# Kernel tuning notes

Measured on AMD Instinct MI355X. Metric: run time of the kernel, lower is better.

The kernel has to match this reference:

```python
import jax, jax.numpy as jnp
import numpy as np

IN_DIM, HID_DIM, OUT_DIM = 1024, 2048, 1024
DEG1, DEG2 = 8, 8
BATCH = 16384


def cheby_kan_layer(x, coeffs):
    """x: [b, i]; coeffs: [i, o, d+1] -> [b, o].
    Per-feature min-max normalize over batch to [-1,1], Chebyshev recurrence, contract."""
    degree = coeffs.shape[-1] - 1
    mn = jnp.min(x, axis=0, keepdims=True)
    mx = jnp.max(x, axis=0, keepdims=True)
    x = 2.0 * (x - mn) / (mx - mn) - 1.0
    Ts = [jnp.ones_like(x)]
    if degree > 0:
        Ts.append(x)
    for _ in range(2, degree + 1):
        Ts.append(2.0 * x * Ts[-1] - Ts[-2])
    cheby = jnp.stack(Ts, axis=-1)  # [b, i, d+1]
    return jnp.einsum('bid,iod->bo', cheby, coeffs)


def setup_inputs() -> dict:
    key = jax.random.key(0)
    k1, k2, k3 = jax.random.split(key, 3)
    x = jax.random.normal(k1, (BATCH, IN_DIM), dtype=jnp.float32)
    # kaiming-uniform-ish init for coeffs
    b1 = float(np.sqrt(6.0 / IN_DIM))
    b2 = float(np.sqrt(6.0 / HID_DIM))
    coeffs1 = jax.random.uniform(k2, (IN_DIM, HID_DIM, DEG1 + 1), dtype=jnp.float32, minval=-b1, maxval=b1)
    coeffs2 = jax.random.uniform(k3, (HID_DIM, OUT_DIM, DEG2 + 1), dtype=jnp.float32, minval=-b2, maxval=b2)
    return {"x": x, "coeffs1": coeffs1, "coeffs2": coeffs2}


def reference(x, coeffs1, coeffs2):
    h = cheby_kan_layer(x, coeffs1)
    y = cheby_kan_layer(h, coeffs2)
    return y
```

## Files before the change

### kernel.cpp

```cpp
#include <hip/hip_runtime.h>
#include <hip/hip_bf16.h>
#include <stdint.h>


constexpr int BATCH   = 16384;
constexpr int IN_DIM  = 1024;
constexpr int HID_DIM = 2048;
constexpr int OUT_DIM = 1024;
#define DP1 9

using bf16_t = __hip_bfloat16;

typedef __attribute__((ext_vector_type(4))) float f32x4;
typedef __attribute__((ext_vector_type(8))) short s16x8;
typedef __attribute__((ext_vector_type(16))) float f32x16;
typedef __attribute__((ext_vector_type(16))) __bf16 bf16x16;

static __device__ __forceinline__ unsigned int f2bf_u(float f) {
  union { __hip_bfloat16 h; unsigned short u; } cv;
  cv.h = __float2bfloat16(f);
  return (unsigned int)cv.u;
}

template <typename T>
__global__ void kan_minmax_partial(const T* __restrict__ x, int rows, int cols,
                                   float* __restrict__ mnp, float* __restrict__ mxp) {
  const int c  = blockIdx.x * 64 + (threadIdx.x & 63);
  const int rg = threadIdx.x >> 6;
  const int P  = gridDim.y;
  const int chunk = rows / P;
  const int r0 = blockIdx.y * chunk;
  float mn = 1e30f, mx = -1e30f;
  for (int r = r0 + rg; r < r0 + chunk; r += 4) {
    float v = (float)x[(size_t)r * cols + c];
    mn = fminf(mn, v); mx = fmaxf(mx, v);
  }
  __shared__ float smn[256], smx[256];
  smn[threadIdx.x] = mn; smx[threadIdx.x] = mx;
  __syncthreads();
  if (rg == 0) {
    int t = threadIdx.x;
    mn = fminf(fminf(smn[t], smn[t + 64]), fminf(smn[t + 128], smn[t + 192]));
    mx = fmaxf(fmaxf(smx[t], smx[t + 64]), fmaxf(smx[t + 128], smx[t + 192]));
    mnp[(size_t)blockIdx.y * cols + c] = mn;
    mxp[(size_t)blockIdx.y * cols + c] = mx;
  }
}

__global__ void kan_minmax_finalize(const float* __restrict__ mnp, const float* __restrict__ mxp,
                                    int cols, int P, float* __restrict__ s, float* __restrict__ t) {
  int c = blockIdx.x * blockDim.x + threadIdx.x;
  if (c >= cols) return;
  float mn = 1e30f, mx = -1e30f;
  for (int p = 0; p < P; ++p) {
    mn = fminf(mn, mnp[(size_t)p * cols + c]);
    mx = fmaxf(mx, mxp[(size_t)p * cols + c]);
  }
  float inv = 2.0f / (mx - mn);
  s[c] = inv;
  t[c] = -mn * inv - 1.0f;
}

__global__ void kan_repack(const float* __restrict__ coeffs, int I, int O,
                           bf16_t* __restrict__ Bp) {
  const int NIB = I / 32;
  const int ib = blockIdx.x % NIB;
  const int ntile = blockIdx.x / NIB;
  const size_t slab0 = (size_t)(ntile * NIB + ib) * 9 * 8192;
  for (int c = threadIdx.x; c < 1024; c += 256) {
    const int l16  = c & 15;
    const int quad = (c >> 4) & 3;
    const int ng   = c >> 6;
    const int o = ntile * 256 + ng * 16 + l16;
    const int ibase = ib * 32 + quad * 8;
    float v[8][9];
#pragma unroll
    for (int q = 0; q < 8; ++q) {
      const float* rp = coeffs + ((size_t)(ibase + q) * O + o) * DP1;
#pragma unroll
      for (int d = 0; d < 9; ++d) v[q][d] = rp[d];
    }
#pragma unroll
    for (int d = 0; d < 9; ++d) {
      unsigned int pk[4];
#pragma unroll
      for (int q = 0; q < 4; ++q)
        pk[q] = f2bf_u(v[2 * q][d]) | (f2bf_u(v[2 * q + 1][d]) << 16);
      *reinterpret_cast<uint4*>(reinterpret_cast<char*>(Bp) +
          (slab0 + (size_t)d * 8192 + (size_t)c * 8) * 2) =
          make_uint4(pk[0], pk[1], pk[2], pk[3]);
    }
  }
}

template <typename AT, typename OT>
__launch_bounds__(256, 2)
__global__ void kan_cheby_gemm(const AT* __restrict__ X, const bf16_t* __restrict__ Bp,
                               const float* __restrict__ sc, const float* __restrict__ tc,
                               OT* __restrict__ out, int I, int N) {
  __shared__ __align__(16) short Als[2][4096];
  __shared__ __align__(16) short Bls[2][8192];

  const int m0   = blockIdx.x * 128;
  const int tid  = threadIdx.x;
  const int lane = tid & 63;
  const int wave = tid >> 6;
  const int wr   = wave >> 1;
  const int wc   = wave & 1;
  const int wm4  = wr * 4;
  const int wn16 = wc * 8;
  const int quad = lane >> 4;
  const int l16  = lane & 15;

  const int ma = tid & 127;
  const int hf = tid >> 7;

  const int NIB = I / 32;
  const int nstage = NIB * 9;
  const size_t slab_base = (size_t)blockIdx.y * NIB * 9 * 8192;

  auto dma_b = [&](int ss) {
    const char* g = reinterpret_cast<const char*>(Bp + slab_base + (size_t)ss * 8192) +
                    wave * 4096 + lane * 16;
    char* l = reinterpret_cast<char*>(&Bls[ss & 1][0]) + wave * 4096;
#pragma unroll
    for (int t = 0; t < 4; ++t)
      __builtin_amdgcn_global_load_lds(
          (const __attribute__((address_space(1))) void*)(g + t * 1024),
          (__attribute__((address_space(3))) void*)(l + t * 1024), 16, 0, 0);
  };

  uint4 rq[4];
  auto load_raw = [&](int ibx) {
    const char* xp = reinterpret_cast<const char*>(
        X + (size_t)(m0 + ma) * I + ibx * 32 + hf * 16);
    if constexpr (sizeof(AT) == 4) {
      rq[0] = *reinterpret_cast<const uint4*>(xp +  0);
      rq[1] = *reinterpret_cast<const uint4*>(xp + 16);
      rq[2] = *reinterpret_cast<const uint4*>(xp + 32);
      rq[3] = *reinterpret_cast<const uint4*>(xp + 48);
    } else {
      rq[0] = *reinterpret_cast<const uint4*>(xp +  0);
      rq[1] = *reinterpret_cast<const uint4*>(xp + 16);
    }
  };

  f32x16 xv, Tm1, Tm2;
#pragma unroll
  for (int j = 0; j < 16; ++j) { xv[j] = 0.f; Tm1[j] = 0.f; Tm2[j] = 0.f; }

  auto unpack_norm = [&](int ibx) {
    const int fbase = ibx * 32 + hf * 16;
    float rv[16];
    const unsigned int* w = reinterpret_cast<const unsigned int*>(rq);
    if constexpr (sizeof(AT) == 4) {
#pragma unroll
      for (int j = 0; j < 16; ++j) rv[j] = __uint_as_float(w[j]);
    } else {
#pragma unroll
      for (int q = 0; q < 8; ++q) {
        rv[2 * q + 0] = __uint_as_float(w[q] << 16);
        rv[2 * q + 1] = __uint_as_float(w[q] & 0xffff0000u);
      }
    }
    const float4* sp = reinterpret_cast<const float4*>(sc + fbase);
    const float4* tp = reinterpret_cast<const float4*>(tc + fbase);
#pragma unroll
    for (int v = 0; v < 4; ++v) {
      float4 s4 = sp[v], t4 = tp[v];
      xv[4 * v + 0] = fmaf(rv[4 * v + 0], s4.x, t4.x);
      xv[4 * v + 1] = fmaf(rv[4 * v + 1], s4.y, t4.y);
      xv[4 * v + 2] = fmaf(rv[4 * v + 2], s4.z, t4.z);
      xv[4 * v + 3] = fmaf(rv[4 * v + 3], s4.w, t4.w);
    }
  };

  auto write_a = [&](int buf, const f32x16& tv) {
    union { bf16x16 v; uint4 q[2]; } u;
    u.v = __builtin_convertvector(tv, bf16x16);
    char* b = reinterpret_cast<char*>(&Als[buf][0]) +
              (ma >> 4) * 1024 + hf * 512 + (ma & 15) * 16;
    *reinterpret_cast<uint4*>(b)       = u.q[0];
    *reinterpret_cast<uint4*>(b + 256) = u.q[1];
  };

  f32x4 acc[4][8] = {};

  load_raw(0);
  dma_b(0);
  {
    f32x16 ones;
#pragma unroll
    for (int j = 0; j < 16; ++j) ones[j] = 1.0f;
    write_a(0, ones);
    Tm1 = ones;
  }
  __syncthreads();

  int dn = 1, ibn = 0;
  for (int s = 0; s < nstage; ++s) {
    if (s + 1 < nstage) {
      dma_b(s + 1);
      f32x16 tv;
      if (dn == 0) {
#pragma unroll
        for (int j = 0; j < 16; ++j) tv[j] = 1.0f;
      } else if (dn == 1) {
        unpack_norm(ibn);
        if (ibn + 1 < NIB) load_raw(ibn + 1);
        tv = xv;
      } else {
        tv = 2.0f * xv * Tm1 - Tm2;
      }
      Tm2 = Tm1; Tm1 = tv;
      write_a((s + 1) & 1, tv);
      if (++dn == DP1) { dn = 0; ++ibn; }
    }

    {
      const char* Ab = reinterpret_cast<const char*>(&Als[s & 1][0]) + lane * 16;
      const char* Bb = reinterpret_cast<const char*>(&Bls[s & 1][0]) + lane * 16;
      s16x8 fa[4], fb[8];
#pragma unroll
      for (int mt = 0; mt < 4; ++mt)
        fa[mt] = *reinterpret_cast<const s16x8*>(Ab + (wm4 + mt) * 1024);
#pragma unroll
      for (int nt = 0; nt < 8; ++nt)
        fb[nt] = *reinterpret_cast<const s16x8*>(Bb + (wn16 + nt) * 1024);
#pragma unroll
      for (int mt = 0; mt < 4; ++mt)
#pragma unroll
        for (int nt = 0; nt < 8; ++nt)
          acc[mt][nt] = __builtin_amdgcn_mfma_f32_16x16x32_bf16(
              fa[mt], fb[nt], acc[mt][nt], 0, 0, 0);
    }

    __syncthreads();
  }

  const int n0 = blockIdx.y * 256;
#pragma unroll
  for (int mt = 0; mt < 4; ++mt) {
#pragma unroll
    for (int nt = 0; nt < 8; ++nt) {
      const int n = n0 + wc * 128 + nt * 16 + l16;
#pragma unroll
      for (int r = 0; r < 4; ++r) {
        const int m = m0 + wr * 64 + mt * 16 + quad * 4 + r;
        float v = acc[mt][nt][r];
        if constexpr (sizeof(OT) == 4)
          out[(size_t)m * N + n] = v;
        else
          out[(size_t)m * N + n] = __float2bfloat16(v);
      }
    }
  }
}

extern "C" void kernel_launch(void* const* d_in, const int* in_sizes, int n_in,
                              void* d_out, int out_size, void* d_ws, size_t ws_size,
                              hipStream_t stream) {
  const float* x  = (const float*)d_in[0];
  const float* c1 = (const float*)d_in[1];
  const float* c2 = (const float*)d_in[2];
  float* out = (float*)d_out;

  char* ws = (char*)d_ws;
  size_t off = 0;
  auto take = [&](size_t n) -> char* {
    char* p = ws + off;
    off += (n + 255) & ~(size_t)255;
    return p;
  };
  bf16_t* Bp1 = (bf16_t*)take((size_t)HID_DIM * IN_DIM  * DP1 * 2);
  bf16_t* Bp2 = (bf16_t*)take((size_t)OUT_DIM * HID_DIM * DP1 * 2);
  bf16_t* h   = (bf16_t*)take((size_t)BATCH * HID_DIM * 2);
  float* s1  = (float*)take(IN_DIM  * 4);
  float* t1  = (float*)take(IN_DIM  * 4);
  float* s2  = (float*)take(HID_DIM * 4);
  float* t2  = (float*)take(HID_DIM * 4);
  float* mnp = (float*)take((size_t)16 * HID_DIM * 4);
  float* mxp = (float*)take((size_t)16 * HID_DIM * 4);

  kan_minmax_partial<float><<<dim3(IN_DIM / 64, 16), 256, 0, stream>>>(x, BATCH, IN_DIM, mnp, mxp);
  kan_minmax_finalize<<<dim3(IN_DIM / 256), 256, 0, stream>>>(mnp, mxp, IN_DIM, 16, s1, t1);
  kan_repack<<<dim3((HID_DIM / 256) * (IN_DIM / 32)), 256, 0, stream>>>(c1, IN_DIM, HID_DIM, Bp1);
  kan_repack<<<dim3((OUT_DIM / 256) * (HID_DIM / 32)), 256, 0, stream>>>(c2, HID_DIM, OUT_DIM, Bp2);
  kan_cheby_gemm<float, bf16_t><<<dim3(BATCH / 128, HID_DIM / 256), 256, 0, stream>>>(
      x, Bp1, s1, t1, h, IN_DIM, HID_DIM);

  kan_minmax_partial<bf16_t><<<dim3(HID_DIM / 64, 16), 256, 0, stream>>>(h, BATCH, HID_DIM, mnp, mxp);
  kan_minmax_finalize<<<dim3(HID_DIM / 256), 256, 0, stream>>>(mnp, mxp, HID_DIM, 16, s2, t2);
  kan_cheby_gemm<bf16_t, float><<<dim3(BATCH / 128, OUT_DIM / 256), 256, 0, stream>>>(
      h, Bp2, s2, t2, out, HID_DIM, OUT_DIM);
}
```

Measured before the change: 1.881 ms.

## Triple-buffer B tiles with deeper prefetch and precise vmcnt waits

Moves the B-tile LDS staging from double to triple buffering, so the async global-to-LDS load is issued two stages ahead. The full __syncthreads is replaced by explicit s_waitcnt vmcnt/lgkmcnt counts plus a raw barrier, so the in-flight prefetch no longer has to drain every stage. MFMA issue priority is also raised around the compute block. This costs extra LDS, which may limit occupancy, and the hand-counted vmcnt values are fragile if the compiler reorders or changes the load counts.

Measured after the change: 2.007 ms. +6.7%, slower.

```diff
diff --git a/kernel.cpp b/kernel.cpp
--- a/kernel.cpp
+++ b/kernel.cpp
@@ -15,6 +15,9 @@
 typedef __attribute__((ext_vector_type(8))) short s16x8;
 typedef __attribute__((ext_vector_type(16))) float f32x16;
 typedef __attribute__((ext_vector_type(16))) __bf16 bf16x16;
+
+#define WAITV(N) asm volatile("s_waitcnt vmcnt(" #N ")" ::: "memory")
+#define WAITL()  asm volatile("s_waitcnt lgkmcnt(0)" ::: "memory")
 
 static __device__ __forceinline__ unsigned int f2bf_u(float f) {
   union { __hip_bfloat16 h; unsigned short u; } cv;
@@ -99,7 +102,7 @@
                                const float* __restrict__ sc, const float* __restrict__ tc,
                                OT* __restrict__ out, int I, int N) {
   __shared__ __align__(16) short Als[2][4096];
-  __shared__ __align__(16) short Bls[2][8192];
+  __shared__ __align__(16) short Bls[3][8192];
 
   const int m0   = blockIdx.x * 128;
   const int tid  = threadIdx.x;
@@ -119,10 +122,10 @@
   const int nstage = NIB * 9;
   const size_t slab_base = (size_t)blockIdx.y * NIB * 9 * 8192;
 
-  auto dma_b = [&](int ss) {
+  auto dma_b = [&](int ss, int buf) {
     const char* g = reinterpret_cast<const char*>(Bp + slab_base + (size_t)ss * 8192) +
                     wave * 4096 + lane * 16;
-    char* l = reinterpret_cast<char*>(&Bls[ss & 1][0]) + wave * 4096;
+    char* l = reinterpret_cast<char*>(&Bls[buf][0]) + wave * 4096;
 #pragma unroll
     for (int t = 0; t < 4; ++t)
       __builtin_amdgcn_global_load_lds(
@@ -187,7 +190,8 @@
   f32x4 acc[4][8] = {};
 
   load_raw(0);
-  dma_b(0);
+  dma_b(0, 0);
+  dma_b(1, 1);
   {
     f32x16 ones;
 #pragma unroll
@@ -195,19 +199,27 @@
     write_a(0, ones);
     Tm1 = ones;
   }
-  __syncthreads();
+  WAITV(4);
+  WAITL();
+  __builtin_amdgcn_s_barrier();
 
   int dn = 1, ibn = 0;
+  int cb = 0, nb = 2;
   for (int s = 0; s < nstage; ++s) {
-    if (s + 1 < nstage) {
-      dma_b(s + 1);
+    const bool have1 = (s + 1 < nstage);
+    const bool have2 = (s + 2 < nstage);
+
+    if (have2) dma_b(s + 2, nb);
+
+    bool did_raw = false;
+    if (have1) {
       f32x16 tv;
       if (dn == 0) {
 #pragma unroll
         for (int j = 0; j < 16; ++j) tv[j] = 1.0f;
       } else if (dn == 1) {
         unpack_norm(ibn);
-        if (ibn + 1 < NIB) load_raw(ibn + 1);
+        if (ibn + 1 < NIB) { load_raw(ibn + 1); did_raw = true; }
         tv = xv;
       } else {
         tv = 2.0f * xv * Tm1 - Tm2;
@@ -219,7 +231,7 @@
 
     {
       const char* Ab = reinterpret_cast<const char*>(&Als[s & 1][0]) + lane * 16;
-      const char* Bb = reinterpret_cast<const char*>(&Bls[s & 1][0]) + lane * 16;
+      const char* Bb = reinterpret_cast<const char*>(&Bls[cb][0]) + lane * 16;
       s16x8 fa[4], fb[8];
 #pragma unroll
       for (int mt = 0; mt < 4; ++mt)
@@ -227,15 +239,31 @@
 #pragma unroll
       for (int nt = 0; nt < 8; ++nt)
         fb[nt] = *reinterpret_cast<const s16x8*>(Bb + (wn16 + nt) * 1024);
+      __builtin_amdgcn_s_setprio(1);
 #pragma unroll
       for (int mt = 0; mt < 4; ++mt)
 #pragma unroll
         for (int nt = 0; nt < 8; ++nt)
           acc[mt][nt] = __builtin_amdgcn_mfma_f32_16x16x32_bf16(
               fa[mt], fb[nt], acc[mt][nt], 0, 0, 0);
-    }
-
-    __syncthreads();
+      __builtin_amdgcn_s_setprio(0);
+    }
+
+    if (have1) {
+      if (have2) {
+        if (did_raw) {
+          if constexpr (sizeof(AT) == 4) WAITV(8); else WAITV(6);
+        } else {
+          WAITV(4);
+        }
+      } else {
+        WAITV(0);
+      }
+      WAITL();
+      __builtin_amdgcn_s_barrier();
+    }
+    cb = (cb == 2) ? 0 : cb + 1;
+    nb = (nb == 2) ? 0 : nb + 1;
   }
 
   const int n0 = blockIdx.y * 256;
```

## Fold degree-0 Chebyshev term into per-output bias to shrink GEMM K

Applied to the files above, without the earlier changes.

The T0=1 term contributes sum_i coeffs[i,o,0] to every output, so the repack kernel now sums those coefficients into a per-output bias and drops degree 0 from the packed B matrix. This cuts the GEMM K dimension from 9 to 8 stages per input block. The bias is added in the epilogue, and the scale/shift vectors are staged in LDS. LDS fragment loads are also hoisted ahead of the A-tile computation. The change adds an extra small reduction kernel, and the bias sum is now in fp32 where it was previously rounded to bf16 per term.

Measured after the change: 1.913 ms. Within noise of the previous version (+1.7%).

```diff
diff --git a/kernel.cpp b/kernel.cpp
--- a/kernel.cpp
+++ b/kernel.cpp
@@ -62,11 +62,12 @@
 }
 
 __global__ void kan_repack(const float* __restrict__ coeffs, int I, int O,
-                           bf16_t* __restrict__ Bp) {
+                           bf16_t* __restrict__ Bp, float* __restrict__ biasp) {
   const int NIB = I / 32;
   const int ib = blockIdx.x % NIB;
   const int ntile = blockIdx.x / NIB;
-  const size_t slab0 = (size_t)(ntile * NIB + ib) * 9 * 8192;
+  const size_t slab0 = (size_t)(ntile * NIB + ib) * 8 * 8192;
+  __shared__ float sb[1024];
   for (int c = threadIdx.x; c < 1024; c += 256) {
     const int l16  = c & 15;
     const int quad = (c >> 4) & 3;
@@ -80,26 +81,50 @@
 #pragma unroll
       for (int d = 0; d < 9; ++d) v[q][d] = rp[d];
     }
-#pragma unroll
-    for (int d = 0; d < 9; ++d) {
+    float bsum = 0.f;
+#pragma unroll
+    for (int q = 0; q < 8; ++q) bsum += v[q][0];
+    sb[c] = bsum;
+#pragma unroll
+    for (int d = 1; d < 9; ++d) {
       unsigned int pk[4];
 #pragma unroll
       for (int q = 0; q < 4; ++q)
         pk[q] = f2bf_u(v[2 * q][d]) | (f2bf_u(v[2 * q + 1][d]) << 16);
       *reinterpret_cast<uint4*>(reinterpret_cast<char*>(Bp) +
-          (slab0 + (size_t)d * 8192 + (size_t)c * 8) * 2) =
+          (slab0 + (size_t)(d - 1) * 8192 + (size_t)c * 8) * 2) =
           make_uint4(pk[0], pk[1], pk[2], pk[3]);
     }
   }
+  __syncthreads();
+  {
+    const int t = threadIdx.x;
+    const int ng = t >> 4, l16 = t & 15;
+    const float s = sb[ng * 64 + l16] + sb[ng * 64 + 16 + l16] +
+                    sb[ng * 64 + 32 + l16] + sb[ng * 64 + 48 + l16];
+    biasp[(size_t)ib * O + ntile * 256 + t] = s;
+  }
+}
+
+__global__ void kan_bias_finalize(const float* __restrict__ biasp, int NIB, int O,
+                                  float* __restrict__ bias) {
+  const int o = blockIdx.x * blockDim.x + threadIdx.x;
+  if (o >= O) return;
+  float s = 0.f;
+  for (int p = 0; p < NIB; ++p) s += biasp[(size_t)p * O + o];
+  bias[o] = s;
 }
 
 template <typename AT, typename OT>
 __launch_bounds__(256, 2)
 __global__ void kan_cheby_gemm(const AT* __restrict__ X, const bf16_t* __restrict__ Bp,
                                const float* __restrict__ sc, const float* __restrict__ tc,
+                               const float* __restrict__ bias,
                                OT* __restrict__ out, int I, int N) {
   __shared__ __align__(16) short Als[2][4096];
   __shared__ __align__(16) short Bls[2][8192];
+  __shared__ __align__(16) float scl[2048];
+  __shared__ __align__(16) float tcl[2048];
 
   const int m0   = blockIdx.x * 128;
   const int tid  = threadIdx.x;
@@ -116,8 +141,8 @@
   const int hf = tid >> 7;
 
   const int NIB = I / 32;
-  const int nstage = NIB * 9;
-  const size_t slab_base = (size_t)blockIdx.y * NIB * 9 * 8192;
+  const int nstage = NIB * 8;
+  const size_t slab_base = (size_t)blockIdx.y * NIB * 8 * 8192;
 
   auto dma_b = [&](int ss) {
     const char* g = reinterpret_cast<const char*>(Bp + slab_base + (size_t)ss * 8192) +
@@ -163,8 +188,8 @@
         rv[2 * q + 1] = __uint_as_float(w[q] & 0xffff0000u);
       }
     }
-    const float4* sp = reinterpret_cast<const float4*>(sc + fbase);
-    const float4* tp = reinterpret_cast<const float4*>(tc + fbase);
+    const float4* sp = reinterpret_cast<const float4*>(&scl[fbase]);
+    const float4* tp = reinterpret_cast<const float4*>(&tcl[fbase]);
 #pragma unroll
     for (int v = 0; v < 4; ++v) {
       float4 s4 = sp[v], t4 = tp[v];
@@ -186,59 +211,63 @@
 
   f32x4 acc[4][8] = {};
 
+  for (int k = tid; k < I; k += 256) { scl[k] = sc[k]; tcl[k] = tc[k]; }
   load_raw(0);
   dma_b(0);
-  {
-    f32x16 ones;
-#pragma unroll
-    for (int j = 0; j < 16; ++j) ones[j] = 1.0f;
-    write_a(0, ones);
-    Tm1 = ones;
-  }
   __syncthreads();
-
-  int dn = 1, ibn = 0;
+  unpack_norm(0);
+  write_a(0, xv);
+  Tm1 = xv;
+#pragma unroll
+  for (int j = 0; j < 16; ++j) Tm2[j] = 1.0f;
+  if (NIB > 1) load_raw(1);
+  __syncthreads();
+
   for (int s = 0; s < nstage; ++s) {
+    if (s + 1 < nstage) dma_b(s + 1);
+
+    const char* Ab = reinterpret_cast<const char*>(&Als[s & 1][0]) + lane * 16;
+    const char* Bb = reinterpret_cast<const char*>(&Bls[s & 1][0]) + lane * 16;
+    s16x8 fa[4], fb[8];
+#pragma unroll
+    for (int mt = 0; mt < 4; ++mt)
+      fa[mt] = *reinterpret_cast<const s16x8*>(Ab + (wm4 + mt) * 1024);
+#pragma unroll
+    for (int nt = 0; nt < 8; ++nt)
+      fb[nt] = *reinterpret_cast<const s16x8*>(Bb + (wn16 + nt) * 1024);
+
     if (s + 1 < nstage) {
-      dma_b(s + 1);
+      const int t = s + 1;
       f32x16 tv;
-      if (dn == 0) {
-#pragma unroll
-        for (int j = 0; j < 16; ++j) tv[j] = 1.0f;
-      } else if (dn == 1) {
+      if ((t & 7) == 0) {
+        const int ibn = t >> 3;
         unpack_norm(ibn);
         if (ibn + 1 < NIB) load_raw(ibn + 1);
-        tv = xv;
+        tv = Tm1 = xv;
+#pragma unroll
+        for (int j = 0; j < 16; ++j) Tm2[j] = 1.0f;
       } else {
         tv = 2.0f * xv * Tm1 - Tm2;
+        Tm2 = Tm1; Tm1 = tv;
       }
-      Tm2 = Tm1; Tm1 = tv;
-      write_a((s + 1) & 1, tv);
-      if (++dn == DP1) { dn = 0; ++ibn; }
-    }
-
-    {
-      const char* Ab = reinterpret_cast<const char*>(&Als[s & 1][0]) + lane * 16;
-      const char* Bb = reinterpret_cast<const char*>(&Bls[s & 1][0]) + lane * 16;
-      s16x8 fa[4], fb[8];
-#pragma unroll
-      for (int mt = 0; mt < 4; ++mt)
-        fa[mt] = *reinterpret_cast<const s16x8*>(Ab + (wm4 + mt) * 1024);
+      write_a(t & 1, tv);
+    }
+
+#pragma unroll
+    for (int mt = 0; mt < 4; ++mt)
 #pragma unroll
       for (int nt = 0; nt < 8; ++nt)
-        fb[nt] = *reinterpret_cast<const s16x8*>(Bb + (wn16 + nt) * 1024);
-#pragma unroll
-      for (int mt = 0; mt < 4; ++mt)
-#pragma unroll
-        for (int nt = 0; nt < 8; ++nt)
-          acc[mt][nt] = __builtin_amdgcn_mfma_f32_16x16x32_bf16(
-              fa[mt], fb[nt], acc[mt][nt], 0, 0, 0);
-    }
+        acc[mt][nt] = __builtin_amdgcn_mfma_f32_16x16x32_bf16(
+            fa[mt], fb[nt], acc[mt][nt], 0, 0, 0);
 
     __syncthreads();
   }
 
   const int n0 = blockIdx.y * 256;
+  float bv[8];
+#pragma unroll
+  for (int nt = 0; nt < 8; ++nt)
+    bv[nt] = bias[n0 + wc * 128 + nt * 16 + l16];
 #pragma unroll
   for (int mt = 0; mt < 4; ++mt) {
 #pragma unroll
@@ -247,7 +276,7 @@
 #pragma unroll
       for (int r = 0; r < 4; ++r) {
         const int m = m0 + wr * 64 + mt * 16 + quad * 4 + r;
-        float v = acc[mt][nt][r];
+        float v = acc[mt][nt][r] + bv[nt];
         if constexpr (sizeof(OT) == 4)
           out[(size_t)m * N + n] = v;
         else
@@ -272,25 +301,31 @@
     off += (n + 255) & ~(size_t)255;
     return p;
   };
-  bf16_t* Bp1 = (bf16_t*)take((size_t)HID_DIM * IN_DIM  * DP1 * 2);
-  bf16_t* Bp2 = (bf16_t*)take((size_t)OUT_DIM * HID_DIM * DP1 * 2);
+  bf16_t* Bp1 = (bf16_t*)take((size_t)HID_DIM * IN_DIM  * 8 * 2);
+  bf16_t* Bp2 = (bf16_t*)take((size_t)OUT_DIM * HID_DIM * 8 * 2);
   bf16_t* h   = (bf16_t*)take((size_t)BATCH * HID_DIM * 2);
   float* s1  = (float*)take(IN_DIM  * 4);
   float* t1  = (float*)take(IN_DIM  * 4);
   float* s2  = (float*)take(HID_DIM * 4);
   float* t2  = (float*)take(HID_DIM * 4);
+  float* b1  = (float*)take(HID_DIM * 4);
+  float* b2  = (float*)take(OUT_DIM * 4);
+  float* bp1 = (float*)take((size_t)(IN_DIM / 32)  * HID_DIM * 4);
+  float* bp2 = (float*)take((size_t)(HID_DIM / 32) * OUT_DIM * 4);
   float* mnp = (float*)take((size_t)16 * HID_DIM * 4);
   float* mxp = (float*)take((size_t)16 * HID_DIM * 4);
 
   kan_minmax_partial<float><<<dim3(IN_DIM / 64, 16), 256, 0, stream>>>(x, BATCH, IN_DIM, mnp, mxp);
   kan_minmax_finalize<<<dim3(IN_DIM / 256), 256, 0, stream>>>(mnp, mxp, IN_DIM, 16, s1, t1);
-  kan_repack<<<dim3((HID_DIM / 256) * (IN_DIM / 32)), 256, 0, stream>>>(c1, IN_DIM, HID_DIM, Bp1);
-  kan_repack<<<dim3((OUT_DIM / 256) * (HID_DIM / 32)), 256, 0, stream>>>(c2, HID_DIM, OUT_DIM, Bp2);
+  kan_repack<<<dim3((HID_DIM / 256) * (IN_DIM / 32)), 256, 0, stream>>>(c1, IN_DIM, HID_DIM, Bp1, bp1);
+  kan_bias_finalize<<<dim3(HID_DIM / 256), 256, 0, stream>>>(bp1, IN_DIM / 32, HID_DIM, b1);
+  kan_repack<<<dim3((OUT_DIM / 256) * (HID_DIM / 32)), 256, 0, stream>>>(c2, HID_DIM, OUT_DIM, Bp2, bp2);
+  kan_bias_finalize<<<dim3(OUT_DIM / 256), 256, 0, stream>>>(bp2, HID_DIM / 32, OUT_DIM, b2);
   kan_cheby_gemm<float, bf16_t><<<dim3(BATCH / 128, HID_DIM / 256), 256, 0, stream>>>(
-      x, Bp1, s1, t1, h, IN_DIM, HID_DIM);
+      x, Bp1, s1, t1, b1, h, IN_DIM, HID_DIM);
 
   kan_minmax_partial<bf16_t><<<dim3(HID_DIM / 64, 16), 256, 0, stream>>>(h, BATCH, HID_DIM, mnp, mxp);
   kan_minmax_finalize<<<dim3(HID_DIM / 256), 256, 0, stream>>>(mnp, mxp, HID_DIM, 16, s2, t2);
   kan_cheby_gemm<bf16_t, float><<<dim3(BATCH / 128, OUT_DIM / 256), 256, 0, stream>>>(
-      h, Bp2, s2, t2, out, HID_DIM, OUT_DIM);
-}
+      h, Bp2, s2, t2, b2, out, HID_DIM, OUT_DIM);
+}
```
